# Kernel optimization log

Measured on AMD Instinct MI355X. Metric: run time of the kernel, lower is better.

Reference implementation:

```python
import jax, jax.numpy as jnp
import numpy as np
import math

DENOM = 32.0

# e3nn scalar_activation normalizes the activation to unit second moment under N(0,1).
# Compute the gelu normalization constant by Gauss-Hermite quadrature.
_zs, _ws = np.polynomial.hermite_e.hermegauss(64)
_g = 0.5 * _zs * (1.0 + np.array([math.erf(z / math.sqrt(2.0)) for z in _zs]))
C_GELU = float(1.0 / math.sqrt((_ws * _g * _g).sum() / math.sqrt(2.0 * math.pi)))


def _spherical_harmonics(r):
    # r: [E,3] unit vectors. Component-normalized real SH for l=1,2,3.
    x, y, z = r[..., 0], r[..., 1], r[..., 2]
    s3, s5, s15 = math.sqrt(3.0), math.sqrt(5.0), math.sqrt(15.0)
    s7, s105 = math.sqrt(7.0), math.sqrt(105.0)
    s35_8, s21_8 = math.sqrt(35.0 / 8.0), math.sqrt(21.0 / 8.0)
    Y1 = s3 * r                                                     # [E,3]
    Y2 = jnp.stack([s15 * x * y, s15 * y * z, 0.5 * s5 * (3 * z * z - 1),
                    s15 * x * z, 0.5 * s15 * (x * x - y * y)], -1)   # [E,5]
    Y3 = jnp.stack([s35_8 * y * (3 * x * x - y * y), s105 * x * y * z,
                    s21_8 * y * (5 * z * z - 1), 0.5 * s7 * z * (5 * z * z - 3),
                    s21_8 * x * (5 * z * z - 1), 0.5 * s105 * z * (x * x - y * y),
                    s35_8 * x * (x * x - 3 * y * y)], -1)            # [E,7]
    return [Y1, Y2, Y3]


def setup_inputs() -> dict:
    key = jax.random.key(0)
    k = jax.random.split(key, 7)
    N, E, MUL, TMUL = 32768, 1048576, 16, 32
    return {
        "x": jax.random.normal(k[0], (N, MUL), jnp.float32),
        "positions": jax.random.normal(k[1], (N, 3), jnp.float32),
        "W_pre": jax.random.normal(k[2], (4, MUL, TMUL), jnp.float32),
        "W_post": jax.random.normal(k[3], (4, TMUL, TMUL), jnp.float32),
        "W_shortcut": jax.random.normal(k[4], (MUL, TMUL), jnp.float32),
        "senders": jax.random.randint(k[5], (E,), 0, N, jnp.int32),
        "receivers": jax.random.randint(k[6], (E,), 0, N, jnp.int32),
    }


def reference(x, positions, W_pre, W_post, W_shortcut, senders, receivers):
    N, mul = x.shape
    tmul = W_pre.shape[-1]
    # --- edge update: sh of relative positions, tensor product with sender scalars ---
    rvec = positions[receivers] - positions[senders]                 # [E,3]
    n = jnp.linalg.norm(rvec, axis=-1, keepdims=True)
    rhat = rvec / jnp.where(n == 0, 1.0, n)
    Ys = _spherical_harmonics(rhat)
    s = x[senders]                                                   # [E,mul] (0e)
    # --- aggregate edge features at receivers (segment sum) ---
    agg = [jax.ops.segment_sum(s, receivers, num_segments=N)]        # 0e block
    for Y in Ys:
        e = (s[:, :, None] * Y[:, None, :]).reshape(s.shape[0], -1)  # 0e x l -> l
        agg.append(jax.ops.segment_sum(e, receivers, num_segments=N).reshape(N, mul, Y.shape[-1]))
    # --- node update: linear_pre -> scalar act -> linear_post, plus shortcut ---
    inv_in = 1.0 / math.sqrt(mul)
    inv_mid = 1.0 / math.sqrt(tmul)
    out = []
    for l in range(4):
        a = agg[l] / DENOM
        if l == 0:
            p = (a @ W_pre[0]) * inv_in
            p = C_GELU * jax.nn.gelu(p, approximate=False)           # act on 0e scalars only
            q = (p @ W_post[0]) * inv_mid
            q = q + (x @ W_shortcut) * inv_in                        # shortcut: only 0e path exists
            out.append(q)
        else:
            p = jnp.einsum('nui,uv->nvi', a, W_pre[l]) * inv_in
            q = jnp.einsum('nvi,vw->nwi', p, W_post[l]) * inv_mid
            out.append(q.reshape(N, -1))
    return jnp.concatenate(out, axis=-1)                              # [N, tmul*16]
```

## Files before the change

### kernel.cpp

```cpp
#include <hip/hip_runtime.h>
#include <math.h>

#define NN 32768
#define EN 1048576
#define NBIN 1024
#define BINCAP 2048
#define TILE 2048

#define C_GELU_F 1.5335262f

__global__ __launch_bounds__(512) void bin_k(const int* __restrict__ snd,
                                             const int* __restrict__ rcv,
                                             const float* __restrict__ pos,
                                             float4* __restrict__ posw,
                                             int* __restrict__ bin_cur,
                                             unsigned* __restrict__ binbuf) {
    __shared__ unsigned cnt[NBIN];
    __shared__ unsigned excl[NBIN];
    __shared__ unsigned cur2[NBIN];
    __shared__ unsigned gbase[NBIN];
    __shared__ unsigned stage[TILE];
    int t = threadIdx.x;
    int tile = blockIdx.x * TILE;
    cnt[t] = 0; cnt[t + 512] = 0; cur2[t] = 0; cur2[t + 512] = 0;
    if (t < 64) {
        int n = (blockIdx.x << 6) + t;
        posw[n] = make_float4(pos[3*n], pos[3*n+1], pos[3*n+2], 0.f);
    }
    __syncthreads();

    unsigned w[TILE / 512];
#pragma unroll
    for (int i = 0; i < TILE / 512; ++i) {
        int e = tile + i * 512 + t;
        unsigned r = (unsigned)rcv[e], s = (unsigned)snd[e];
        w[i] = (r << 15) | s;
        atomicAdd(&cnt[w[i] >> 20], 1u);
    }
    __syncthreads();

    unsigned my0 = cnt[t], my1 = cnt[t + 512];
    excl[t] = my0; excl[t + 512] = my1;
    __syncthreads();
    for (int d = 1; d < NBIN; d <<= 1) {
        unsigned v0 = (t >= d) ? excl[t - d] : 0u;
        unsigned v1 = excl[t + 512 - d];
        __syncthreads();
        excl[t] += v0; excl[t + 512] += v1;
        __syncthreads();
    }
    gbase[t]       = atomicAdd((unsigned*)&bin_cur[t], my0);
    gbase[t + 512] = atomicAdd((unsigned*)&bin_cur[t + 512], my1);
    excl[t] -= my0; excl[t + 512] -= my1;
    __syncthreads();

#pragma unroll
    for (int i = 0; i < TILE / 512; ++i) {
        unsigned b = w[i] >> 20;
        unsigned p = excl[b] + atomicAdd(&cur2[b], 1u);
        stage[p] = w[i];
    }
    __syncthreads();

    for (int p = t; p < TILE; p += 512) {
        unsigned ww = stage[p];
        unsigned b = ww >> 20;
        unsigned idx = gbase[b] + ((unsigned)p - excl[b]);
        if (idx < BINCAP) binbuf[b * BINCAP + idx] = ww;
    }
}

#define GROUPS 32
#define BLK 512
#define YST 20
#define GST (16*YST + 8)

__global__ __launch_bounds__(512, 4) void fused_k(const float* __restrict__ x,
                                                  const float4* __restrict__ posw,
                                                  const int* __restrict__ bin_cur,
                                                  const unsigned* __restrict__ binbuf,
                                                  const float* __restrict__ Wpre,
                                                  const float* __restrict__ Wpost,
                                                  const float* __restrict__ Wsc,
                                                  float* __restrict__ out) {
    __shared__ float sPre[4*516];
    __shared__ float sPost[4*1028];
    __shared__ float sSc[512];
    __shared__ float sY[GROUPS * GST];
    __shared__ unsigned short sEdge[BINCAP];
    __shared__ unsigned sCnt[32];
    __shared__ unsigned sExcl[32];
    __shared__ unsigned sCur[32];

    int t = threadIdx.x;
    int b = blockIdx.x;

    for (int idx = t; idx < 2048; idx += BLK)
        sPre[(idx >> 9)*516 + (idx & 511)] = Wpre[idx];
    for (int idx = t; idx < 4096; idx += BLK)
        sPost[(idx >> 10)*1028 + (idx & 1023)] = Wpost[idx];
    sSc[t] = Wsc[t];
    if (t < 32) { sCnt[t] = 0; sCur[t] = 0; }

    int M = bin_cur[b]; M = M > BINCAP ? BINCAP : M;
    unsigned* sRaw = (unsigned*)sY;
    __syncthreads();

    for (int i = t; i < M; i += BLK) {
        unsigned ww = binbuf[b * BINCAP + i];
        sRaw[i] = ww;
        atomicAdd(&sCnt[(ww >> 15) & 31], 1u);
    }
    __syncthreads();
    if (t < 32) {
        unsigned val = sCnt[t];
        unsigned inc = val;
#pragma unroll
        for (int d = 1; d < 32; d <<= 1) {
            unsigned v = __shfl_up(inc, d, 32);
            if (t >= d) inc += v;
        }
        sExcl[t] = inc - val;
    }
    __syncthreads();
    for (int i = t; i < M; i += BLK) {
        unsigned ww = sRaw[i];
        unsigned r5 = (ww >> 15) & 31;
        unsigned dst = sExcl[r5] + atomicAdd(&sCur[r5], 1u);
        sEdge[dst] = (unsigned short)(ww & 0x7FFF);
    }
    __syncthreads();

    int g = t >> 4;
    int j = t & 15;
    int n = (b << 5) + g;
    int beg = (int)sExcl[g];
    int cnt = (int)sCnt[g];
    float4 rp = posw[n];
    float* yg = sY + g * GST;

    const float s3   = 1.7320508075688772f;
    const float s5   = 2.2360679774997896f;
    const float s15  = 3.8729833462074170f;
    const float s7   = 2.6457513110645907f;
    const float s105 = 10.246950765959598f;
    const float s35_8 = 2.0916500663351889f;
    const float s21_8 = 1.6201851746019651f;

    float acc[16];
#pragma unroll
    for (int u = 0; u < 16; ++u) acc[u] = 0.f;

    int nch = (cnt + 15) >> 4;
    if (nch > 0) {
        int ki0 = (j < cnt) ? j : cnt - 1;
        int sE = (int)sEdge[beg + ki0];
        float4 sp = posw[sE];

        for (int c = 0; c < nch; ++c) {
            int kn = ((c + 1) << 4) + j;
            int kiN = (kn < cnt) ? kn : cnt - 1;
            int sEn = (int)sEdge[beg + kiN];

            float vx = rp.x - sp.x, vy = rp.y - sp.y, vz = rp.z - sp.z;
            float n2 = vx*vx + vy*vy + vz*vz;
            float inv;
            if (n2 > 0.f) {
                inv = rsqrtf(n2);
                inv = inv * (1.5f - 0.5f * n2 * inv * inv);
            } else inv = 0.f;
            float X = vx*inv, Y = vy*inv, Z = vz*inv;
            float XX = X*X, YY = Y*Y, ZZ = Z*Z;
            float m = (((c << 4) + j) < cnt) ? 1.f : 0.f;

            float* yr = yg + j * YST;
            ((float4*)yr)[0] = make_float4(m, m*(s3*X), m*(s3*Y), m*(s3*Z));
            ((float4*)yr)[1] = make_float4(m*(s15*X*Y), m*(s15*Y*Z),
                                           m*(0.5f*s5*(3.f*ZZ - 1.f)), m*(s15*X*Z));
            ((float4*)yr)[2] = make_float4(m*(0.5f*s15*(XX - YY)),
                                           m*(s35_8*Y*(3.f*XX - YY)),
                                           m*(s105*X*Y*Z),
                                           m*(s21_8*Y*(5.f*ZZ - 1.f)));
            ((float4*)yr)[3] = make_float4(m*(0.5f*s7*Z*(5.f*ZZ - 3.f)),
                                           m*(s21_8*X*(5.f*ZZ - 1.f)),
                                           m*(0.5f*s105*Z*(XX - YY)),
                                           m*(s35_8*X*(XX - 3.f*YY)));

            int se[16];
#pragma unroll
            for (int e = 0; e < 16; ++e)
                se[e] = __shfl(sE, (t & 48) + e, 64);
            float yt[16];
#pragma unroll
            for (int e = 0; e < 16; ++e)
                yt[e] = yg[e * YST + j];

            float4 spn = posw[sEn];

#pragma unroll
            for (int e = 0; e < 16; ++e) {
                float y = yt[e];
                const float4* xp = (const float4*)(x + (se[e] << 4));
                float4 a0 = xp[0], a1 = xp[1], a2 = xp[2], a3 = xp[3];
                acc[0]  += a0.x * y;  acc[1]  += a0.y * y;
                acc[2]  += a0.z * y;  acc[3]  += a0.w * y;
                acc[4]  += a1.x * y;  acc[5]  += a1.y * y;
                acc[6]  += a1.z * y;  acc[7]  += a1.w * y;
                acc[8]  += a2.x * y;  acc[9]  += a2.y * y;
                acc[10] += a2.z * y;  acc[11] += a2.w * y;
                acc[12] += a3.x * y;  acc[13] += a3.y * y;
                acc[14] += a3.z * y;  acc[15] += a3.w * y;
            }

            sE = sEn; sp = spn;
        }
    }

    int l, i, offl, deg;
    if (j == 0)      { l = 0; i = 0;     offl = 0;   deg = 1; }
    else if (j < 4)  { l = 1; i = j - 1; offl = 32;  deg = 3; }
    else if (j < 9)  { l = 2; i = j - 4; offl = 128; deg = 5; }
    else             { l = 3; i = j - 9; offl = 288; deg = 7; }

    const float c1 = 0.0078125f;
    const float c2 = 0.17677669529663687f;

    float p[32];
#pragma unroll
    for (int v = 0; v < 32; ++v) p[v] = 0.f;
    const float* wp = sPre + l * 516;
#pragma unroll
    for (int uu = 0; uu < 16; ++uu) {
        float a = acc[uu];
        const float4* w4 = (const float4*)(wp + (uu << 5));
#pragma unroll
        for (int vq = 0; vq < 8; ++vq) {
            float4 w = w4[vq];
            p[4*vq+0] += a * w.x;
            p[4*vq+1] += a * w.y;
            p[4*vq+2] += a * w.z;
            p[4*vq+3] += a * w.w;
        }
    }
#pragma unroll
    for (int v = 0; v < 32; ++v) p[v] *= c1;

    if (j == 0) {
#pragma unroll
        for (int v = 0; v < 32; ++v) {
            float pv = p[v];
            p[v] = C_GELU_F * 0.5f * pv * (1.f + erff(pv * 0.7071067811865476f));
        }
    }

    float q[32];
#pragma unroll
    for (int w = 0; w < 32; ++w) q[w] = 0.f;
    const float* wq = sPost + l * 1028;
#pragma unroll
    for (int v = 0; v < 32; ++v) {
        float pv = p[v];
        const float4* w4 = (const float4*)(wq + (v << 5));
#pragma unroll
        for (int wd = 0; wd < 8; ++wd) {
            float4 w = w4[wd];
            q[4*wd+0] += pv * w.x;
            q[4*wd+1] += pv * w.y;
            q[4*wd+2] += pv * w.z;
            q[4*wd+3] += pv * w.w;
        }
    }
#pragma unroll
    for (int w = 0; w < 32; ++w) q[w] *= c2;

    if (j == 0) {
        const float* xp = x + (n << 4);
#pragma unroll
        for (int uu = 0; uu < 16; ++uu) {
            float xv = 0.25f * xp[uu];
            const float4* w4 = (const float4*)(sSc + (uu << 5));
#pragma unroll
            for (int wd = 0; wd < 8; ++wd) {
                float4 w = w4[wd];
                q[4*wd+0] += xv * w.x;
                q[4*wd+1] += xv * w.y;
                q[4*wd+2] += xv * w.z;
                q[4*wd+3] += xv * w.w;
            }
        }
    }

    float* op = out + (n << 9) + offl + i;
#pragma unroll
    for (int w = 0; w < 32; ++w) op[w * deg] = q[w];
}

extern "C" void kernel_launch(void* const* d_in, const int* in_sizes, int n_in,
                              void* d_out, int out_size, void* d_ws, size_t ws_size,
                              hipStream_t stream) {
    const float* x     = (const float*)d_in[0];
    const float* pos   = (const float*)d_in[1];
    const float* Wpre  = (const float*)d_in[2];
    const float* Wpost = (const float*)d_in[3];
    const float* Wsc   = (const float*)d_in[4];
    const int*   snd   = (const int*)d_in[5];
    const int*   rcv   = (const int*)d_in[6];
    float* out = (float*)d_out;

    char* ws = (char*)d_ws;
    int*      bin_cur   = (int*)(ws);
    float4*   posw      = (float4*)(ws + 0x30000);
    unsigned* binbuf    = (unsigned*)(ws + 0x500000);

    hipMemsetAsync(bin_cur, 0, NBIN * sizeof(int), stream);
    bin_k<<<EN / TILE, 512, 0, stream>>>(snd, rcv, pos, posw, bin_cur, binbuf);
    fused_k<<<NBIN, BLK, 0, stream>>>(x, posw, bin_cur, binbuf,
                                      Wpre, Wpost, Wsc, out);
}
```

Measured before the change: 191.7 us.

## Simplify binning with atomic ranks and sort receivers by degree for balance

The binning kernel now uses the return value of the shared-memory atomic as each edge's rank within its bin. This drops the block-wide prefix scan, the staging buffer and the extra barriers, at the cost of losing locally sorted write order to the global bins. The fused kernel bitonic-sorts the 32 receivers in a block by edge count, so receivers with similar degree share a wavefront and lanes sit idle less often. Sender indices are now read directly from LDS instead of being broadcast with shuffles.

Result: faster. 186.1 us (-2.9%).

```diff
diff --git a/kernel.cpp b/kernel.cpp
--- a/kernel.cpp
+++ b/kernel.cpp
@@ -16,13 +16,10 @@
                                              int* __restrict__ bin_cur,
                                              unsigned* __restrict__ binbuf) {
     __shared__ unsigned cnt[NBIN];
-    __shared__ unsigned excl[NBIN];
-    __shared__ unsigned cur2[NBIN];
     __shared__ unsigned gbase[NBIN];
-    __shared__ unsigned stage[TILE];
     int t = threadIdx.x;
     int tile = blockIdx.x * TILE;
-    cnt[t] = 0; cnt[t + 512] = 0; cur2[t] = 0; cur2[t + 512] = 0;
+    cnt[t] = 0; cnt[t + 512] = 0;
     if (t < 64) {
         int n = (blockIdx.x << 6) + t;
         posw[n] = make_float4(pos[3*n], pos[3*n+1], pos[3*n+2], 0.f);
@@ -30,43 +27,24 @@
     __syncthreads();
 
     unsigned w[TILE / 512];
+    unsigned rk[TILE / 512];
 #pragma unroll
     for (int i = 0; i < TILE / 512; ++i) {
         int e = tile + i * 512 + t;
         unsigned r = (unsigned)rcv[e], s = (unsigned)snd[e];
         w[i] = (r << 15) | s;
-        atomicAdd(&cnt[w[i] >> 20], 1u);
-    }
-    __syncthreads();
-
-    unsigned my0 = cnt[t], my1 = cnt[t + 512];
-    excl[t] = my0; excl[t + 512] = my1;
-    __syncthreads();
-    for (int d = 1; d < NBIN; d <<= 1) {
-        unsigned v0 = (t >= d) ? excl[t - d] : 0u;
-        unsigned v1 = excl[t + 512 - d];
-        __syncthreads();
-        excl[t] += v0; excl[t + 512] += v1;
-        __syncthreads();
-    }
-    gbase[t]       = atomicAdd((unsigned*)&bin_cur[t], my0);
-    gbase[t + 512] = atomicAdd((unsigned*)&bin_cur[t + 512], my1);
-    excl[t] -= my0; excl[t + 512] -= my1;
+        rk[i] = atomicAdd(&cnt[w[i] >> 20], 1u);
+    }
+    __syncthreads();
+    gbase[t]       = atomicAdd((unsigned*)&bin_cur[t],       cnt[t]);
+    gbase[t + 512] = atomicAdd((unsigned*)&bin_cur[t + 512], cnt[t + 512]);
     __syncthreads();
 
 #pragma unroll
     for (int i = 0; i < TILE / 512; ++i) {
         unsigned b = w[i] >> 20;
-        unsigned p = excl[b] + atomicAdd(&cur2[b], 1u);
-        stage[p] = w[i];
-    }
-    __syncthreads();
-
-    for (int p = t; p < TILE; p += 512) {
-        unsigned ww = stage[p];
-        unsigned b = ww >> 20;
-        unsigned idx = gbase[b] + ((unsigned)p - excl[b]);
-        if (idx < BINCAP) binbuf[b * BINCAP + idx] = ww;
+        unsigned idx = gbase[b] + rk[i];
+        if (idx < BINCAP) binbuf[b * BINCAP + idx] = w[i];
     }
 }
 
@@ -91,6 +69,7 @@
     __shared__ unsigned sCnt[32];
     __shared__ unsigned sExcl[32];
     __shared__ unsigned sCur[32];
+    __shared__ unsigned sPerm[32];
 
     int t = threadIdx.x;
     int b = blockIdx.x;
@@ -121,6 +100,20 @@
             if (t >= d) inc += v;
         }
         sExcl[t] = inc - val;
+
+        unsigned key = (val << 5) | (unsigned)t;
+#pragma unroll
+        for (int k = 2; k <= 32; k <<= 1) {
+#pragma unroll
+            for (int j2 = k >> 1; j2 > 0; j2 >>= 1) {
+                unsigned o = __shfl_xor(key, j2, 32);
+                bool lower = (t & j2) == 0;
+                bool up = (t & k) == 0;
+                bool take = (key > o) != (lower != up);
+                key = take ? o : key;
+            }
+        }
+        sPerm[t] = key & 31u;
     }
     __syncthreads();
     for (int i = t; i < M; i += BLK) {
@@ -133,9 +126,10 @@
 
     int g = t >> 4;
     int j = t & 15;
-    int n = (b << 5) + g;
-    int beg = (int)sExcl[g];
-    int cnt = (int)sCnt[g];
+    int rId = (int)sPerm[g];
+    int n = (b << 5) + rId;
+    int beg = (int)sExcl[rId];
+    int cnt = (int)sCnt[rId];
     float4 rp = posw[n];
     float* yg = sY + g * GST;
 
@@ -153,14 +147,14 @@
 
     int nch = (cnt + 15) >> 4;
     if (nch > 0) {
-        int ki0 = (j < cnt) ? j : cnt - 1;
-        int sE = (int)sEdge[beg + ki0];
-        float4 sp = posw[sE];
+        int last = cnt - 1;
+        int k0 = j < last ? j : last;
+        int sA = (int)sEdge[beg + k0];
+        float4 sp = posw[sA];
 
         for (int c = 0; c < nch; ++c) {
-            int kn = ((c + 1) << 4) + j;
-            int kiN = (kn < cnt) ? kn : cnt - 1;
-            int sEn = (int)sEdge[beg + kiN];
+            int kn = ((c + 1) << 4) + j; kn = kn < last ? kn : last;
+            int sAn = (int)sEdge[beg + kn];
 
             float vx = rp.x - sp.x, vy = rp.y - sp.y, vz = rp.z - sp.z;
             float n2 = vx*vx + vy*vy + vz*vz;
@@ -188,14 +182,17 @@
 
             int se[16];
 #pragma unroll
-            for (int e = 0; e < 16; ++e)
-                se[e] = __shfl(sE, (t & 48) + e, 64);
+            for (int e = 0; e < 16; ++e) {
+                int idx = (c << 4) + e;
+                idx = idx < last ? idx : last;
+                se[e] = (int)sEdge[beg + idx];
+            }
             float yt[16];
 #pragma unroll
             for (int e = 0; e < 16; ++e)
                 yt[e] = yg[e * YST + j];
 
-            float4 spn = posw[sEn];
+            float4 spn = posw[sAn];
 
 #pragma unroll
             for (int e = 0; e < 16; ++e) {
@@ -212,7 +209,7 @@
                 acc[14] += a3.z * y;  acc[15] += a3.w * y;
             }
 
-            sE = sEn; sp = spn;
+            sp = spn;
         }
     }
 
```
